# Kernel optimization log

Hardware: AMD Instinct MI355X
Metric: run time of the kernel (lower is better)

## Reference

```python
import jax, jax.numpy as jnp
import numpy as np

# HUSM region -> channel mapping (19 channels, 4 disjoint regions)
REGIONS = [
    [0, 1, 5, 8, 9, 10, 14],    # frontal
    [2, 11, 17],                # central
    [3, 12, 18],                # parietal
    [4, 6, 7, 13, 15, 16],      # occipital
]
N_CHAN = 19
N_REG = 4
_region_id = np.empty(N_CHAN, dtype=np.int32)
for r, chans in enumerate(REGIONS):
    for c in chans:
        _region_id[c] = r
REGION_ID = jnp.array(_region_id)
REGION_COUNTS = jnp.array([len(r) for r in REGIONS], dtype=jnp.float32)

N_HEADS, D_K, D_V, D_MODEL, D_FF = 8, 32, 32, 256, 1024
EPS = 1e-5


def layernorm(x):
    # default nn.LayerNorm: gamma=1, beta=0 (layer re-created each forward)
    mu = jnp.mean(x, axis=-1, keepdims=True)
    var = jnp.var(x, axis=-1, keepdims=True)
    return (x - mu) * jax.lax.rsqrt(var + EPS)


def mha(q_in, k_in, v_in, wq, wk, wv, wo):
    # q_in: [B, S, D]
    B, S, _ = q_in.shape
    Q = jnp.einsum('bsd,dhk->bhsk', q_in, wq.reshape(D_MODEL, N_HEADS, D_K))
    K = jnp.einsum('bsd,dhk->bhsk', k_in, wk.reshape(D_MODEL, N_HEADS, D_K))
    V = jnp.einsum('bsd,dhv->bhsv', v_in, wv.reshape(D_MODEL, N_HEADS, D_V))
    scores = jnp.einsum('bhqk,bhsk->bhqs', Q, K) / jnp.sqrt(jnp.float32(D_K))
    attn = jax.nn.softmax(scores, axis=-1)
    ctx = jnp.einsum('bhqs,bhsv->bqhv', attn, V).reshape(B, S, N_HEADS * D_V)
    return layernorm(ctx @ wo + q_in)


def setup_inputs() -> dict:
    key = jax.random.key(0)
    ks = jax.random.split(key, 12)
    B = 4096
    sc = 1.0 / np.sqrt(D_MODEL)
    inp = {
        'x': jax.random.normal(ks[0], (B, N_CHAN, D_MODEL), dtype=jnp.float32),
        'rsa_wq': jax.random.normal(ks[1], (D_MODEL, D_MODEL), dtype=jnp.float32) * sc,
        'rsa_wk': jax.random.normal(ks[2], (D_MODEL, D_MODEL), dtype=jnp.float32) * sc,
        'rsa_wv': jax.random.normal(ks[3], (D_MODEL, D_MODEL), dtype=jnp.float32) * sc,
        'rsa_wo': jax.random.normal(ks[4], (D_MODEL, D_MODEL), dtype=jnp.float32) * sc,
        'lsa_wq': jax.random.normal(ks[5], (D_MODEL, D_MODEL), dtype=jnp.float32) * sc,
        'lsa_wk': jax.random.normal(ks[6], (D_MODEL, D_MODEL), dtype=jnp.float32) * sc,
        'lsa_wv': jax.random.normal(ks[7], (D_MODEL, D_MODEL), dtype=jnp.float32) * sc,
        'lsa_wo': jax.random.normal(ks[8], (D_MODEL, D_MODEL), dtype=jnp.float32) * sc,
        'ffn_w1': jax.random.normal(ks[9], (D_MODEL, D_FF), dtype=jnp.float32) * sc,
        'ffn_w2': jax.random.normal(ks[10], (D_FF, D_MODEL), dtype=jnp.float32) * (1.0 / np.sqrt(D_FF)),
    }
    return inp


def reference(x, rsa_wq, rsa_wk, rsa_wv, rsa_wo,
              lsa_wq, lsa_wk, lsa_wv, lsa_wo, ffn_w1, ffn_w2):
    # --- region gather + avgpool: mean of channels per region -> [B, 4, D]
    fe_sum = jax.ops.segment_sum(jnp.swapaxes(x, 0, 1), REGION_ID,
                                 num_segments=N_REG)          # [4, B, D]
    fe_region = jnp.swapaxes(fe_sum, 0, 1) / REGION_COUNTS[None, :, None]
    # --- tiny 4-token region self-attention
    refined = mha(fe_region, fe_region, fe_region,
                  rsa_wq, rsa_wk, rsa_wv, rsa_wo)             # [B, 4, D]
    # --- scatter-add refined region feature back to its channels
    x = x + refined[:, REGION_ID, :]                          # [B, 19, D]
    # --- full-channel MHA + FFN
    fused = mha(x, x, x, lsa_wq, lsa_wk, lsa_wv, lsa_wo)
    ffn = jax.nn.relu(fused @ ffn_w1) @ ffn_w2
    return layernorm(ffn + fused)
```

## Files before the change

### kernel.cpp

```cpp
#include <hip/hip_runtime.h>
#include <stdint.h>
#include <stddef.h>


#define DEVINL __device__ __forceinline__

typedef __attribute__((ext_vector_type(8))) short short8;
typedef __attribute__((ext_vector_type(4))) float floatx4;
typedef __attribute__((ext_vector_type(8))) unsigned short ushort8;
typedef __attribute__((ext_vector_type(4))) unsigned short ushort4v;

DEVINL float bf2f(unsigned short u){
  union { unsigned int i; float f; } x; x.i = ((unsigned int)u) << 16; return x.f;
}
DEVINL unsigned short f2bf(float f){
  union { float f; unsigned int i; } x; x.f = f;
  unsigned int r = x.i + 0x7fffu + ((x.i >> 16) & 1u);
  return (unsigned short)(r >> 16);
}

typedef __attribute__((address_space(1))) void gvoid_t;
typedef __attribute__((address_space(3))) void lvoid_t;
DEVINL void gload_lds16(const void* g, void* l){
  __builtin_amdgcn_global_load_lds((gvoid_t*)g, (lvoid_t*)l, 16, 0, 0);
}

__global__ __launch_bounds__(256) void wprep_all(
    const float* __restrict__ rq, const float* __restrict__ rk,
    const float* __restrict__ rv, const float* __restrict__ ro,
    const float* __restrict__ lq, const float* __restrict__ lk,
    const float* __restrict__ lv, const float* __restrict__ lo,
    const float* __restrict__ w1, const float* __restrict__ w2,
    unsigned short* __restrict__ wt)
{
  int idx = blockIdx.x * 256 + threadIdx.x;
  const float* W; unsigned short* D; int N, r;
  const int K = (idx < 786432) ? 256 : 1024;
  if (idx < 524288){
    int wsel = idx >> 16; r = idx & 65535; N = 256; D = wt + wsel * 65536;
    switch (wsel){
      case 0: W = rq; break; case 1: W = rk; break; case 2: W = rv; break; case 3: W = ro; break;
      case 4: W = lq; break; case 5: W = lk; break; case 6: W = lv; break; default: W = lo; break;
    }
  } else if (idx < 786432){
    r = idx - 524288; N = 1024; D = wt + 524288; W = w1;
  } else {
    r = idx - 786432; N = 256; D = wt + 786432; W = w2;
  }
  int k = r / N, n = r - k * N;
  D[(size_t)n * K + k] = f2bf(W[r]);
}

__global__ __launch_bounds__(256) void pool_kernel(const float* __restrict__ x,
                                                   unsigned short* __restrict__ fe)
{
  const int b = blockIdx.x, d = threadIdx.x;
  const float* xb = x + (size_t)b * 4864 + d;
  float s0 = xb[0*256]+xb[1*256]+xb[5*256]+xb[8*256]+xb[9*256]+xb[10*256]+xb[14*256];
  float s1 = xb[2*256]+xb[11*256]+xb[17*256];
  float s2 = xb[3*256]+xb[12*256]+xb[18*256];
  float s3 = xb[4*256]+xb[6*256]+xb[7*256]+xb[13*256]+xb[15*256]+xb[16*256];
  unsigned short* fb = fe + (size_t)b * 1024 + d;
  fb[0]   = f2bf(s0 * (1.f/7.f));
  fb[256] = f2bf(s1 * (1.f/3.f));
  fb[512] = f2bf(s2 * (1.f/3.f));
  fb[768] = f2bf(s3 * (1.f/6.f));
}

template<int RELU, int SPLIT, int NPAN>
__global__ __launch_bounds__(256, 3)
void gemm_kernel(const unsigned short* __restrict__ A,
                 const unsigned short* __restrict__ Bt,
                 unsigned short* __restrict__ C0,
                 unsigned short* __restrict__ C1,
                 unsigned short* __restrict__ C2,
                 int M, int N, int K)
{
  __shared__ __align__(1024) unsigned short lds[2][8192];
  const int tid  = threadIdx.x;
  const int wave = tid >> 6, lane = tid & 63;
  const int wm = wave >> 1, wn = wave & 1;

  const int nwg = gridDim.x;
  const int o = blockIdx.x;
  const int g = ((o & 7) * (nwg >> 3)) + (o >> 3);
  const int rowA0 = (g / NPAN) * 128;
  const int rowB0 = (g % NPAN) * 128;

  const int stg_row = lane >> 3;
  const int stg_kb  = (((lane & 7) ^ (lane >> 3)) << 4);

  floatx4 acc[4][4];
  #pragma unroll
  for (int i = 0; i < 4; ++i)
    #pragma unroll
    for (int j = 0; j < 4; ++j) acc[i][j] = (floatx4){0.f, 0.f, 0.f, 0.f};

  const int nk = K >> 6;
  for (int kt = 0; kt < nk; ++kt){
    if (kt) __syncthreads();
    const int kbase = kt << 7;
    #pragma unroll
    for (int s = 0; s < 4; ++s){
      int chunk = wave * 4 + s;
      int r = chunk * 8 + stg_row;
      gload_lds16((const char*)(A  + (size_t)(rowA0 + r) * K) + kbase + stg_kb,
                  (char*)(&lds[0][0]) + chunk * 1024);
      gload_lds16((const char*)(Bt + (size_t)(rowB0 + r) * K) + kbase + stg_kb,
                  (char*)(&lds[1][0]) + chunk * 1024);
    }
    __syncthreads();
    const char* As = (const char*)(&lds[0][0]);
    const char* Bs = (const char*)(&lds[1][0]);
    #pragma unroll
    for (int kk = 0; kk < 2; ++kk){
      short8 a[4], b[4];
      #pragma unroll
      for (int i = 0; i < 4; ++i){
        int row = wm * 64 + i * 16 + (lane & 15);
        int kb  = (kk * 64 + ((lane >> 4) << 4)) ^ ((row & 7) << 4);
        a[i] = *(const short8*)(As + row * 128 + kb);
      }
      #pragma unroll
      for (int j = 0; j < 4; ++j){
        int row = wn * 64 + j * 16 + (lane & 15);
        int kb  = (kk * 64 + ((lane >> 4) << 4)) ^ ((row & 7) << 4);
        b[j] = *(const short8*)(Bs + row * 128 + kb);
      }
      #pragma unroll
      for (int i = 0; i < 4; ++i)
        #pragma unroll
        for (int j = 0; j < 4; ++j)
          acc[i][j] = __builtin_amdgcn_mfma_f32_16x16x32_bf16(a[i], b[j], acc[i][j], 0, 0, 0);
    }
  }

  unsigned short* dst;
  int colb, ldc;
  if (SPLIT){
    const int seg = rowB0 >> 8;
    dst = (seg == 0) ? C0 : (seg == 1) ? C1 : C2;
    colb = rowB0 & 255;
    ldc = 256;
  } else {
    dst = C0; colb = rowB0; ldc = N;
  }
  const int cr = (lane >> 4) << 2;
  const int cc = lane & 15;
  #pragma unroll
  for (int i = 0; i < 4; ++i){
    #pragma unroll
    for (int j = 0; j < 4; ++j){
      int r0 = rowA0 + wm * 64 + i * 16 + cr;
      int c0 = colb + wn * 64 + j * 16 + cc;
      #pragma unroll
      for (int r = 0; r < 4; ++r){
        float v = acc[i][j][r];
        if (RELU) v = fmaxf(v, 0.f);
        dst[(size_t)(r0 + r) * ldc + c0] = f2bf(v);
      }
    }
  }
}

template<int OUTF32>
__global__ __launch_bounds__(512, 4)
void gemm_ln_kernel(const unsigned short* __restrict__ A,
                    const unsigned short* __restrict__ Bt,
                    const unsigned short* __restrict__ Res,
                    void* __restrict__ Out, int M, int K)
{
  __shared__ __align__(1024) char lds[2][40960];
  const int tid  = threadIdx.x;
  const int wave = tid >> 6, lane = tid & 63;
  const int wm = wave >> 2, wn = wave & 3;
  const int rowA0 = blockIdx.x * 64;
  const int stg_row = lane >> 3;
  const int stg_kb  = (((lane & 7) ^ (lane >> 3)) << 4);

  floatx4 acc[2][4];
  #pragma unroll
  for (int i = 0; i < 2; ++i)
    #pragma unroll
    for (int j = 0; j < 4; ++j) acc[i][j] = (floatx4){0.f, 0.f, 0.f, 0.f};

  const int nk = K >> 6;
  int cur = 0;
  #pragma unroll
  for (int s = 0; s < 5; ++s){
    int chunk = wave * 5 + s;
    const unsigned short* src = (chunk < 8)
      ? A  + (size_t)(rowA0 + chunk * 8 + stg_row) * K
      : Bt + (size_t)((chunk - 8) * 8 + stg_row) * K;
    gload_lds16((const char*)src + stg_kb, &lds[0][0] + chunk * 1024);
  }
  __syncthreads();

  for (int kt = 0; kt < nk; ++kt){
    if (kt + 1 < nk){
      const int kbase = (kt + 1) << 7;
      #pragma unroll
      for (int s = 0; s < 5; ++s){
        int chunk = wave * 5 + s;
        const unsigned short* src = (chunk < 8)
          ? A  + (size_t)(rowA0 + chunk * 8 + stg_row) * K
          : Bt + (size_t)((chunk - 8) * 8 + stg_row) * K;
        gload_lds16((const char*)src + kbase + stg_kb, &lds[cur ^ 1][0] + chunk * 1024);
      }
    }
    const char* As = &lds[cur][0];
    const char* Bs = &lds[cur][0] + 8192;
    #pragma unroll
    for (int kk = 0; kk < 2; ++kk){
      short8 a[2], b[4];
      #pragma unroll
      for (int i = 0; i < 2; ++i){
        int row = wm * 32 + i * 16 + (lane & 15);
        int kb  = (kk * 64 + ((lane >> 4) << 4)) ^ ((row & 7) << 4);
        a[i] = *(const short8*)(As + row * 128 + kb);
      }
      #pragma unroll
      for (int j = 0; j < 4; ++j){
        int row = wn * 64 + j * 16 + (lane & 15);
        int kb  = (kk * 64 + ((lane >> 4) << 4)) ^ ((row & 7) << 4);
        b[j] = *(const short8*)(Bs + row * 128 + kb);
      }
      #pragma unroll
      for (int i = 0; i < 2; ++i)
        #pragma unroll
        for (int j = 0; j < 4; ++j)
          acc[i][j] = __builtin_amdgcn_mfma_f32_16x16x32_bf16(a[i], b[j], acc[i][j], 0, 0, 0);
    }
    __syncthreads();
    cur ^= 1;
  }

  float* red_s = (float*)&lds[0][0];
  float* red_q = red_s + 256;
  float* mu_a  = red_s + 512;
  float* rs_a  = red_s + 576;
  const int g  = lane >> 4;
  const int cl = lane & 15;
  #pragma unroll
  for (int i = 0; i < 2; ++i){
    #pragma unroll
    for (int r = 0; r < 4; ++r){
      const int rowl = wm * 32 + i * 16 + g * 4 + r;
      float s = 0.f, q = 0.f;
      #pragma unroll
      for (int j = 0; j < 4; ++j){
        float v = acc[i][j][r] +
                  bf2f(Res[(size_t)(rowA0 + rowl) * 256 + wn * 64 + j * 16 + cl]);
        acc[i][j][r] = v;
        s += v; q += v * v;
      }
      #pragma unroll
      for (int off = 1; off < 16; off <<= 1){
        s += __shfl_xor(s, off); q += __shfl_xor(q, off);
      }
      if (cl == 0){ red_s[wn * 64 + rowl] = s; red_q[wn * 64 + rowl] = q; }
    }
  }
  __syncthreads();
  if (tid < 64){
    float S = red_s[tid] + red_s[64 + tid] + red_s[128 + tid] + red_s[192 + tid];
    float Q = red_q[tid] + red_q[64 + tid] + red_q[128 + tid] + red_q[192 + tid];
    float mu = S * (1.f / 256.f);
    float var = Q * (1.f / 256.f) - mu * mu;
    mu_a[tid] = mu;
    rs_a[tid] = rsqrtf(var + 1e-5f);
  }
  __syncthreads();
  #pragma unroll
  for (int i = 0; i < 2; ++i){
    #pragma unroll
    for (int r = 0; r < 4; ++r){
      const int rowl = wm * 32 + i * 16 + g * 4 + r;
      const float mu = mu_a[rowl], rs = rs_a[rowl];
      #pragma unroll
      for (int j = 0; j < 4; ++j){
        float w = (acc[i][j][r] - mu) * rs;
        size_t idx = (size_t)(rowA0 + rowl) * 256 + wn * 64 + j * 16 + cl;
        if (OUTF32) ((float*)Out)[idx] = w;
        else        ((unsigned short*)Out)[idx] = f2bf(w);
      }
    }
  }
}

__global__ __launch_bounds__(256) void attn4_kernel(
    const unsigned short* __restrict__ Q, const unsigned short* __restrict__ K,
    const unsigned short* __restrict__ V, unsigned short* __restrict__ ctx)
{
  const int t = threadIdx.x;
  const int lb = t >> 5, u = t & 31, h = u >> 2, q = u & 3;
  const size_t b = (size_t)blockIdx.x * 8 + lb;
  const size_t base = b * 1024 + h * 32;

  float qf[32];
  {
    const ushort8* qp = (const ushort8*)(Q + base + q * 256);
    #pragma unroll
    for (int g = 0; g < 4; ++g){
      ushort8 v = qp[g];
      #pragma unroll
      for (int e = 0; e < 8; ++e) qf[g * 8 + e] = bf2f(v[e]);
    }
  }
  float sc[4];
  #pragma unroll
  for (int s = 0; s < 4; ++s){
    const ushort8* kp = (const ushort8*)(K + base + s * 256);
    float a0 = 0, a1 = 0, a2 = 0, a3 = 0;
    #pragma unroll
    for (int g = 0; g < 4; ++g){
      ushort8 v = kp[g];
      a0 += qf[g*8+0]*bf2f(v[0]); a1 += qf[g*8+1]*bf2f(v[1]);
      a2 += qf[g*8+2]*bf2f(v[2]); a3 += qf[g*8+3]*bf2f(v[3]);
      a0 += qf[g*8+4]*bf2f(v[4]); a1 += qf[g*8+5]*bf2f(v[5]);
      a2 += qf[g*8+6]*bf2f(v[6]); a3 += qf[g*8+7]*bf2f(v[7]);
    }
    sc[s] = ((a0 + a1) + (a2 + a3)) * 0.17677669529663687f;
  }
  float m = fmaxf(fmaxf(sc[0], sc[1]), fmaxf(sc[2], sc[3]));
  float sum = 0.f;
  #pragma unroll
  for (int s = 0; s < 4; ++s){ sc[s] = __expf(sc[s] - m); sum += sc[s]; }
  float inv = 1.f / sum;

  float o[32];
  #pragma unroll
  for (int d = 0; d < 32; ++d) o[d] = 0.f;
  #pragma unroll
  for (int s = 0; s < 4; ++s){
    float p = sc[s] * inv;
    const ushort8* vp = (const ushort8*)(V + base + s * 256);
    #pragma unroll
    for (int g = 0; g < 4; ++g){
      ushort8 v = vp[g];
      #pragma unroll
      for (int e = 0; e < 8; ++e) o[g * 8 + e] += p * bf2f(v[e]);
    }
  }
  unsigned short* cp = ctx + base + q * 256;
  #pragma unroll
  for (int g = 0; g < 4; ++g){
    ushort8 w;
    #pragma unroll
    for (int e = 0; e < 8; ++e) w[e] = f2bf(o[g * 8 + e]);
    ((ushort8*)cp)[g] = w;
  }
}

__global__ __launch_bounds__(256) void scatter_kernel(
    const float* __restrict__ x, const unsigned short* __restrict__ ref,
    unsigned short* __restrict__ x2)
{
  const int b = blockIdx.x, t = threadIdx.x;
  const int d0 = (t & 63) * 4;
  const int cbase = t >> 6;
  float rv[4][4];
  #pragma unroll
  for (int r = 0; r < 4; ++r){
    ushort4v rr = *(const ushort4v*)(ref + (size_t)b * 1024 + r * 256 + d0);
    #pragma unroll
    for (int e = 0; e < 4; ++e) rv[r][e] = bf2f(rr[e]);
  }
  const unsigned long long packed = 0x27CE40F390ull;
  #pragma unroll
  for (int k = 0; k < 5; ++k){
    int c = cbase + k * 4;
    if (c < 19){
      int r = (int)((packed >> (2 * c)) & 3ull);
      floatx4 xv = *(const floatx4*)(x + (size_t)b * 4864 + c * 256 + d0);
      ushort4v w;
      #pragma unroll
      for (int e = 0; e < 4; ++e) w[e] = f2bf(xv[e] + rv[r][e]);
      *(ushort4v*)(x2 + (size_t)b * 4864 + c * 256 + d0) = w;
    }
  }
}

__global__ __launch_bounds__(256) void attn19_kernel(
    const unsigned short* __restrict__ Q, const unsigned short* __restrict__ K,
    const unsigned short* __restrict__ V, unsigned short* __restrict__ ctx)
{
  __shared__ float Kl[4864];
  __shared__ float Vl[4864];
  const size_t b = blockIdx.x;
  const unsigned short* Kb = K + b * 4864;
  const unsigned short* Vb = V + b * 4864;
  for (int i = threadIdx.x; i < 4864; i += 256){ Kl[i] = bf2f(Kb[i]); Vl[i] = bf2f(Vb[i]); }
  __syncthreads();
  const int t = threadIdx.x;
  if (t >= 152) return;
  const int h = t / 19, qq = t - h * 19;

  float qf[32];
  {
    const ushort8* qp = (const ushort8*)(Q + b * 4864 + qq * 256 + h * 32);
    #pragma unroll
    for (int g = 0; g < 4; ++g){
      ushort8 v = qp[g];
      #pragma unroll
      for (int e = 0; e < 8; ++e) qf[g * 8 + e] = bf2f(v[e]);
    }
  }
  float p[19];
  float m = -1e30f;
  #pragma unroll
  for (int s = 0; s < 19; ++s){
    const float* kr = &Kl[s * 256 + h * 32];
    float a0 = 0, a1 = 0, a2 = 0, a3 = 0;
    #pragma unroll
    for (int d = 0; d < 32; d += 4){
      a0 += qf[d+0] * kr[d+0]; a1 += qf[d+1] * kr[d+1];
      a2 += qf[d+2] * kr[d+2]; a3 += qf[d+3] * kr[d+3];
    }
    p[s] = ((a0 + a1) + (a2 + a3)) * 0.17677669529663687f;
    m = fmaxf(m, p[s]);
  }
  float sum = 0.f;
  #pragma unroll
  for (int s = 0; s < 19; ++s){ p[s] = __expf(p[s] - m); sum += p[s]; }
  float inv = 1.f / sum;

  float o[32];
  #pragma unroll
  for (int d = 0; d < 32; ++d) o[d] = 0.f;
  #pragma unroll
  for (int s = 0; s < 19; ++s){
    float ps = p[s] * inv;
    const float* vr = &Vl[s * 256 + h * 32];
    #pragma unroll
    for (int d = 0; d < 32; ++d) o[d] += ps * vr[d];
  }
  unsigned short* cp = ctx + b * 4864 + qq * 256 + h * 32;
  #pragma unroll
  for (int g = 0; g < 4; ++g){
    ushort8 w;
    #pragma unroll
    for (int e = 0; e < 8; ++e) w[e] = f2bf(o[g * 8 + e]);
    ((ushort8*)cp)[g] = w;
  }
}

extern "C" void kernel_launch(void* const* d_in, const int* in_sizes, int n_in,
                              void* d_out, int out_size, void* d_ws, size_t ws_size,
                              hipStream_t stream)
{
  (void)n_in; (void)out_size;
  const float* x  = (const float*)d_in[0];
  const float* rq = (const float*)d_in[1];
  const float* rk = (const float*)d_in[2];
  const float* rv = (const float*)d_in[3];
  const float* ro = (const float*)d_in[4];
  const float* lq = (const float*)d_in[5];
  const float* lk = (const float*)d_in[6];
  const float* lv = (const float*)d_in[7];
  const float* lo = (const float*)d_in[8];
  const float* w1 = (const float*)d_in[9];
  const float* w2 = (const float*)d_in[10];

  const int B = in_sizes[0] / 4864;
  const int M4  = B * 4;
  const int M19 = B * 19;
  const int MH  = M19 / 2;
  const size_t MB = 1ull << 20;
  if (ws_size < 240 * MB) return;

  char* ws = (char*)d_ws;
  unsigned short* WT    = (unsigned short*)(ws);
  unsigned short* FE    = (unsigned short*)(ws + 2   * MB);
  unsigned short* Q4    = (unsigned short*)(ws + 10  * MB);
  unsigned short* K4    = (unsigned short*)(ws + 18  * MB);
  unsigned short* V4    = (unsigned short*)(ws + 26  * MB);
  unsigned short* CTX4  = (unsigned short*)(ws + 34  * MB);
  unsigned short* REF   = (unsigned short*)(ws + 42  * MB);
  unsigned short* X2    = (unsigned short*)(ws + 50  * MB);
  unsigned short* Q19   = (unsigned short*)(ws + 88  * MB);
  unsigned short* K19   = (unsigned short*)(ws + 126 * MB);
  unsigned short* V19   = (unsigned short*)(ws + 164 * MB);
  unsigned short* CTX19 = (unsigned short*)(ws + 202 * MB);
  unsigned short* FUSED = (unsigned short*)(ws + 88  * MB);
  unsigned short* H     = (unsigned short*)(ws + 126 * MB);
  float* out = (float*)d_out;

  wprep_all<<<4096, 256, 0, stream>>>(rq, rk, rv, ro, lq, lk, lv, lo, w1, w2, WT);
  pool_kernel<<<B, 256, 0, stream>>>(x, FE);
  gemm_kernel<0,1,6><<<6 * (M4/128), 256, 0, stream>>>(FE, WT, Q4, K4, V4, M4, 768, 256);
  attn4_kernel<<<B/8, 256, 0, stream>>>(Q4, K4, V4, CTX4);
  gemm_ln_kernel<0><<<M4/64, 512, 0, stream>>>(CTX4, WT + 3*65536, FE, REF, M4, 256);
  scatter_kernel<<<B, 256, 0, stream>>>(x, REF, X2);
  gemm_kernel<0,1,6><<<6 * (M19/128), 256, 0, stream>>>(X2, WT + 4*65536, Q19, K19, V19, M19, 768, 256);
  attn19_kernel<<<B, 256, 0, stream>>>(Q19, K19, V19, CTX19);
  gemm_ln_kernel<0><<<M19/64, 512, 0, stream>>>(CTX19, WT + 7*65536, X2, FUSED, M19, 256);
  for (int hf = 0; hf < 2; ++hf){
    const unsigned short* Fh = FUSED + (size_t)hf * MH * 256;
    gemm_kernel<1,0,8><<<8 * (MH/128), 256, 0, stream>>>(Fh, WT + 524288, H, nullptr, nullptr, MH, 1024, 256);
    gemm_ln_kernel<1><<<MH/64, 512, 0, stream>>>(H, WT + 786432, Fh,
                                                 out + (size_t)hf * MH * 256, MH, 1024);
  }
}
```

Measured before the change: 366.9 us.

## Fuse FFN up-projection, ReLU, down-projection and LayerNorm into one kernel

Replaces the two-pass FFN (a GEMM writing the hidden activation H to global memory, then a GEMM+LayerNorm reading it back, done in two halves) with a single kernel per 32-row tile. That kernel keeps the 32x1024 ReLU hidden tile in LDS and runs the second GEMM, residual add and LayerNorm in place. This removes the global write and read of the large hidden tensor and several launches. In exchange the weight B-operands are loaded straight from global memory without LDS staging, and each block uses about 80KB of LDS, which may limit occupancy and add weight traffic.

Measured after the change: 771.8 us. 2.1x slower.

```diff
diff --git a/kernel.cpp b/kernel.cpp
--- a/kernel.cpp
+++ b/kernel.cpp
@@ -284,6 +284,126 @@
         if (OUTF32) ((float*)Out)[idx] = w;
         else        ((unsigned short*)Out)[idx] = f2bf(w);
       }
+    }
+  }
+}
+
+__global__ __launch_bounds__(512, 4)
+void ffn_fused_kernel(const unsigned short* __restrict__ A,
+                      const unsigned short* __restrict__ W1t,
+                      const unsigned short* __restrict__ W2t,
+                      float* __restrict__ Out, int M)
+{
+  __shared__ __align__(1024) unsigned short Al[8192];
+  __shared__ __align__(1024) unsigned short Hl[32768];
+  const int tid  = threadIdx.x;
+  const int wave = tid >> 6, lane = tid & 63;
+  const int wm = wave >> 2, wn = wave & 3;
+  const int rowA0 = blockIdx.x * 32;
+  const int ko = (lane >> 4) << 3;
+
+  const int stg_row = lane >> 3;
+  const int stg_kb  = (((lane & 7) ^ (lane >> 3)) << 4);
+  #pragma unroll
+  for (int s = 0; s < 2; ++s){
+    int c = wave * 2 + s;
+    int p = c >> 2, rg = c & 3;
+    int r = rg * 8 + stg_row;
+    gload_lds16((const char*)(A + (size_t)(rowA0 + r) * 256 + p * 64) + stg_kb,
+                (char*)Al + c * 1024);
+  }
+  __syncthreads();
+
+  short8 af[8];
+  {
+    const int row = wm * 16 + (lane & 15);
+    const int rx = (row & 7) << 4;
+    #pragma unroll
+    for (int kk = 0; kk < 8; ++kk){
+      int kb = (((kk & 1) << 6) + ((lane >> 4) << 4)) ^ rx;
+      af[kk] = *(const short8*)((const char*)Al + (kk >> 1) * 4096 + row * 128 + kb);
+    }
+  }
+
+  const int w1r = wn * 16 + (lane & 15);
+  for (int p = 0; p < 16; ++p){
+    floatx4 acc = (floatx4){0.f, 0.f, 0.f, 0.f};
+    #pragma unroll
+    for (int kk = 0; kk < 8; ++kk){
+      short8 b = *(const short8*)(W1t + (size_t)(p * 64 + w1r) * 256 + kk * 32 + ko);
+      acc = __builtin_amdgcn_mfma_f32_16x16x32_bf16(af[kk], b, acc, 0, 0, 0);
+    }
+    const int hcol = p * 64 + wn * 16 + (lane & 15);
+    #pragma unroll
+    for (int r = 0; r < 4; ++r){
+      const int arow = wm * 16 + ((lane >> 4) << 2) + r;
+      *(unsigned short*)((char*)Hl + arow * 2048 + ((hcol * 2) ^ ((arow & 7) << 4)))
+          = f2bf(fmaxf(acc[r], 0.f));
+    }
+  }
+  __syncthreads();
+
+  floatx4 acc2[4];
+  #pragma unroll
+  for (int j = 0; j < 4; ++j) acc2[j] = (floatx4){0.f, 0.f, 0.f, 0.f};
+  {
+    const int row = wm * 16 + (lane & 15);
+    const int rx = (row & 7) << 4;
+    for (int kk = 0; kk < 32; ++kk){
+      short8 a = *(const short8*)((const char*)Hl + row * 2048 +
+                                  ((kk * 64 + ((lane >> 4) << 4)) ^ rx));
+      #pragma unroll
+      for (int j = 0; j < 4; ++j){
+        short8 b = *(const short8*)(W2t + (size_t)(wn * 64 + j * 16 + (lane & 15)) * 1024
+                                    + kk * 32 + ko);
+        acc2[j] = __builtin_amdgcn_mfma_f32_16x16x32_bf16(a, b, acc2[j], 0, 0, 0);
+      }
+    }
+  }
+  __syncthreads();
+
+  float* red_s = (float*)Hl;
+  float* red_q = red_s + 128;
+  float* mu_a  = red_s + 256;
+  float* rs_a  = red_s + 288;
+  const int g  = lane >> 4;
+  const int cl = lane & 15;
+  #pragma unroll
+  for (int r = 0; r < 4; ++r){
+    const int rowl = wm * 16 + g * 4 + r;
+    float s = 0.f, q = 0.f;
+    #pragma unroll
+    for (int j = 0; j < 4; ++j){
+      const int col = wn * 64 + j * 16 + cl;
+      unsigned short resb = *(const unsigned short*)((const char*)Al + (col >> 6) * 4096
+                              + rowl * 128 + (((col & 63) * 2) ^ ((rowl & 7) << 4)));
+      float v = acc2[j][r] + bf2f(resb);
+      acc2[j][r] = v;
+      s += v; q += v * v;
+    }
+    #pragma unroll
+    for (int off = 1; off < 16; off <<= 1){
+      s += __shfl_xor(s, off); q += __shfl_xor(q, off);
+    }
+    if (cl == 0){ red_s[wn * 32 + rowl] = s; red_q[wn * 32 + rowl] = q; }
+  }
+  __syncthreads();
+  if (tid < 32){
+    float S = red_s[tid] + red_s[32 + tid] + red_s[64 + tid] + red_s[96 + tid];
+    float Q = red_q[tid] + red_q[32 + tid] + red_q[64 + tid] + red_q[96 + tid];
+    float mu = S * (1.f / 256.f);
+    float var = Q * (1.f / 256.f) - mu * mu;
+    mu_a[tid] = mu;
+    rs_a[tid] = rsqrtf(var + 1e-5f);
+  }
+  __syncthreads();
+  #pragma unroll
+  for (int r = 0; r < 4; ++r){
+    const int rowl = wm * 16 + g * 4 + r;
+    const float mu = mu_a[rowl], rs = rs_a[rowl];
+    #pragma unroll
+    for (int j = 0; j < 4; ++j){
+      Out[(size_t)(rowA0 + rowl) * 256 + wn * 64 + j * 16 + cl] = (acc2[j][r] - mu) * rs;
     }
   }
 }
@@ -465,7 +585,6 @@
   const int B = in_sizes[0] / 4864;
   const int M4  = B * 4;
   const int M19 = B * 19;
-  const int MH  = M19 / 2;
   const size_t MB = 1ull << 20;
   if (ws_size < 240 * MB) return;
 
@@ -483,7 +602,6 @@
   unsigned short* V19   = (unsigned short*)(ws + 164 * MB);
   unsigned short* CTX19 = (unsigned short*)(ws + 202 * MB);
   unsigned short* FUSED = (unsigned short*)(ws + 88  * MB);
-  unsigned short* H     = (unsigned short*)(ws + 126 * MB);
   float* out = (float*)d_out;
 
   wprep_all<<<4096, 256, 0, stream>>>(rq, rk, rv, ro, lq, lk, lv, lo, w1, w2, WT);
@@ -495,10 +613,5 @@
   gemm_kernel<0,1,6><<<6 * (M19/128), 256, 0, stream>>>(X2, WT + 4*65536, Q19, K19, V19, M19, 768, 256);
   attn19_kernel<<<B, 256, 0, stream>>>(Q19, K19, V19, CTX19);
   gemm_ln_kernel<0><<<M19/64, 512, 0, stream>>>(CTX19, WT + 7*65536, X2, FUSED, M19, 256);
-  for (int hf = 0; hf < 2; ++hf){
-    const unsigned short* Fh = FUSED + (size_t)hf * MH * 256;
-    gemm_kernel<1,0,8><<<8 * (MH/128), 256, 0, stream>>>(Fh, WT + 524288, H, nullptr, nullptr, MH, 1024, 256);
-    gemm_ln_kernel<1><<<MH/64, 512, 0, stream>>>(H, WT + 786432, Fh,
-                                                 out + (size_t)hf * MH * 256, MH, 1024);
-  }
-}
+  ffn_fused_kernel<<<M19/32, 512, 0, stream>>>(FUSED, WT + 524288, WT + 786432, out, M19);
+}
```

## Pack attn19 threads densely and read K/V directly from global memory

Applied to the files above, without the earlier changes.

The 19-token attention kernel previously ran one block per batch, staged K and V into shared memory as fp32, and left 104 of 256 threads idle. It now assigns one thread per (batch, query, head) across a flat grid, so every lane does work, and reads bf16 K/V rows straight from global memory with 16-byte vector loads, relying on cache hits for reuse across the 19 queries. This removes the LDS staging, the barrier and the shared-memory occupancy limit. In exchange there is more redundant global/L2 traffic, since each query thread rereads the same K/V rows.

After: 408.2 us. 11.3% more time.

```diff
diff --git a/kernel.cpp b/kernel.cpp
--- a/kernel.cpp
+++ b/kernel.cpp
@@ -385,20 +385,17 @@
     const unsigned short* __restrict__ Q, const unsigned short* __restrict__ K,
     const unsigned short* __restrict__ V, unsigned short* __restrict__ ctx)
 {
-  __shared__ float Kl[4864];
-  __shared__ float Vl[4864];
-  const size_t b = blockIdx.x;
-  const unsigned short* Kb = K + b * 4864;
-  const unsigned short* Vb = V + b * 4864;
-  for (int i = threadIdx.x; i < 4864; i += 256){ Kl[i] = bf2f(Kb[i]); Vl[i] = bf2f(Vb[i]); }
-  __syncthreads();
-  const int t = threadIdx.x;
-  if (t >= 152) return;
-  const int h = t / 19, qq = t - h * 19;
+  const int tid = blockIdx.x * 256 + threadIdx.x;
+  const int b = tid / 152;
+  const int r = tid - b * 152;
+  const int q = r >> 3, h = r & 7;
+  const size_t bb = (size_t)b * 4864;
+  const unsigned short* Kb = K + bb + h * 32;
+  const unsigned short* Vb = V + bb + h * 32;
 
   float qf[32];
   {
-    const ushort8* qp = (const ushort8*)(Q + b * 4864 + qq * 256 + h * 32);
+    const ushort8* qp = (const ushort8*)(Q + bb + q * 256 + h * 32);
     #pragma unroll
     for (int g = 0; g < 4; ++g){
       ushort8 v = qp[g];
@@ -406,16 +403,20 @@
       for (int e = 0; e < 8; ++e) qf[g * 8 + e] = bf2f(v[e]);
     }
   }
+
   float p[19];
   float m = -1e30f;
   #pragma unroll
   for (int s = 0; s < 19; ++s){
-    const float* kr = &Kl[s * 256 + h * 32];
+    const ushort8* kp = (const ushort8*)(Kb + s * 256);
     float a0 = 0, a1 = 0, a2 = 0, a3 = 0;
     #pragma unroll
-    for (int d = 0; d < 32; d += 4){
-      a0 += qf[d+0] * kr[d+0]; a1 += qf[d+1] * kr[d+1];
-      a2 += qf[d+2] * kr[d+2]; a3 += qf[d+3] * kr[d+3];
+    for (int g = 0; g < 4; ++g){
+      ushort8 v = kp[g];
+      a0 += qf[g*8+0]*bf2f(v[0]); a1 += qf[g*8+1]*bf2f(v[1]);
+      a2 += qf[g*8+2]*bf2f(v[2]); a3 += qf[g*8+3]*bf2f(v[3]);
+      a0 += qf[g*8+4]*bf2f(v[4]); a1 += qf[g*8+5]*bf2f(v[5]);
+      a2 += qf[g*8+6]*bf2f(v[6]); a3 += qf[g*8+7]*bf2f(v[7]);
     }
     p[s] = ((a0 + a1) + (a2 + a3)) * 0.17677669529663687f;
     m = fmaxf(m, p[s]);
@@ -431,11 +432,15 @@
   #pragma unroll
   for (int s = 0; s < 19; ++s){
     float ps = p[s] * inv;
-    const float* vr = &Vl[s * 256 + h * 32];
-    #pragma unroll
-    for (int d = 0; d < 32; ++d) o[d] += ps * vr[d];
-  }
-  unsigned short* cp = ctx + b * 4864 + qq * 256 + h * 32;
+    const ushort8* vp = (const ushort8*)(Vb + s * 256);
+    #pragma unroll
+    for (int g = 0; g < 4; ++g){
+      ushort8 v = vp[g];
+      #pragma unroll
+      for (int e = 0; e < 8; ++e) o[g * 8 + e] += ps * bf2f(v[e]);
+    }
+  }
+  unsigned short* cp = ctx + bb + q * 256 + h * 32;
   #pragma unroll
   for (int g = 0; g < 4; ++g){
     ushort8 w;
@@ -493,7 +498,7 @@
   gemm_ln_kernel<0><<<M4/64, 512, 0, stream>>>(CTX4, WT + 3*65536, FE, REF, M4, 256);
   scatter_kernel<<<B, 256, 0, stream>>>(x, REF, X2);
   gemm_kernel<0,1,6><<<6 * (M19/128), 256, 0, stream>>>(X2, WT + 4*65536, Q19, K19, V19, M19, 768, 256);
-  attn19_kernel<<<B, 256, 0, stream>>>(Q19, K19, V19, CTX19);
+  attn19_kernel<<<(B * 152) / 256, 256, 0, stream>>>(Q19, K19, V19, CTX19);
   gemm_ln_kernel<0><<<M19/64, 512, 0, stream>>>(CTX19, WT + 7*65536, X2, FUSED, M19, 256);
   for (int hf = 0; hf < 2; ++hf){
     const unsigned short* Fh = FUSED + (size_t)hf * MH * 256;
```
